# Optimization experiments

Hardware: AMD Instinct MI355X
Metric: run time of the kernel (lower is better)

Reference implementation:

```python
import jax, jax.numpy as jnp
import numpy as np

IN_DIM = 4096
OUT_DIM = 4096
RANK = 16
BATCH = 4
SEQ = 2048


def setup_inputs() -> dict:
    key = jax.random.key(0)
    ks = jax.random.split(key, 7)
    x = jax.random.normal(ks[0], (BATCH, SEQ, IN_DIM), dtype=jnp.float32)
    org_weight = jax.random.normal(ks[1], (OUT_DIM, IN_DIM), dtype=jnp.float32) * 0.02
    org_bias = jax.random.normal(ks[2], (OUT_DIM,), dtype=jnp.float32) * 0.02
    hada_w1_a = jax.random.normal(ks[3], (OUT_DIM, RANK), dtype=jnp.float32) * 0.1
    hada_w1_b = jax.random.normal(ks[4], (RANK, IN_DIM), dtype=jnp.float32)
    hada_w2_a = jax.random.normal(ks[5], (OUT_DIM, RANK), dtype=jnp.float32) * 0.1
    hada_w2_b = jax.random.normal(ks[6], (RANK, IN_DIM), dtype=jnp.float32)
    scalar = jnp.ones((), dtype=jnp.float32)
    return {
        "x": x,
        "org_weight": org_weight,
        "org_bias": org_bias,
        "hada_w1_a": hada_w1_a,
        "hada_w1_b": hada_w1_b,
        "hada_w2_a": hada_w2_a,
        "hada_w2_b": hada_w2_b,
        "scalar": scalar,
    }


def reference(x, org_weight, org_bias, hada_w1_a, hada_w1_b, hada_w2_a, hada_w2_b, scalar):
    scale = jnp.asarray(1.0, dtype=hada_w1_b.dtype)   # self.scale = 1.0
    multiplier = jnp.asarray(1.0, dtype=x.dtype)       # self.multiplier = 1.0
    # base = F.linear(x, org_weight, org_bias)
    base = jnp.einsum("bsi,oi->bso", x, org_weight) + org_bias
    # diff_weight = (w1a @ w1b) * (w2a @ w2b) * scale * scalar  -> [out, in]
    diff_weight = (hada_w1_a @ hada_w1_b) * (hada_w2_a @ hada_w2_b) * scale * scalar
    # delta = F.linear(x, diff_weight * multiplier)
    delta = jnp.einsum("bsi,oi->bso", x, diff_weight * multiplier)
    return base + delta
```

## Files before the change

### kernel.cpp

```cpp
#include <hip/hip_runtime.h>

#define IN_DIM 4096
#define OUT_DIM 4096
#define RANK 16
#define MDIM 8192

typedef unsigned short ushort_t;
typedef __attribute__((ext_vector_type(8))) short short8;
typedef __attribute__((ext_vector_type(4))) float floatx4;
typedef __attribute__((ext_vector_type(4))) ushort_t ushort4_t;

__device__ __forceinline__ ushort_t f2b(float f) {
    union { float f; unsigned int i; } v; v.f = f;
    unsigned int u = v.i;
    u += 0x7FFFu + ((u >> 16) & 1u);
    return (ushort_t)(u >> 16);
}

#define GLOAD_LDS16(gp, lp)                                                    \
    __builtin_amdgcn_global_load_lds(                                          \
        (__attribute__((address_space(1))) void*)(gp),                         \
        (__attribute__((address_space(3))) void*)(lp), 16, 0, 0)

__global__ __launch_bounds__(256) void convx_kernel(
    const float4* __restrict__ x, ushort4_t* __restrict__ xb, int n4)
{
    int i = blockIdx.x * blockDim.x + threadIdx.x;
    int stride = gridDim.x * blockDim.x;
    for (; i < n4; i += stride) {
        float4 v = x[i];
        ushort4_t o;
        o.x = f2b(v.x); o.y = f2b(v.y); o.z = f2b(v.z); o.w = f2b(v.w);
        xb[i] = o;
    }
}

__global__ __launch_bounds__(256) void weff_kernel(
    const float* __restrict__ orgw,
    const float* __restrict__ w1a, const float* __restrict__ w1b,
    const float* __restrict__ w2a, const float* __restrict__ w2b,
    const float* __restrict__ scalar,
    ushort_t* __restrict__ weff)
{
    __shared__ float s1b[RANK][256];
    __shared__ float s2b[RANK][256];
    __shared__ float s1a[64 * RANK];
    __shared__ float s2a[64 * RANK];

    const int t  = threadIdx.x;
    const int i0 = blockIdx.x * 256;
    const int o0 = blockIdx.y * 64;

    #pragma unroll
    for (int r = 0; r < RANK; ++r) {
        s1b[r][t] = w1b[r * IN_DIM + i0 + t];
        s2b[r][t] = w2b[r * IN_DIM + i0 + t];
    }
    for (int e = t; e < 64 * RANK; e += 256) {
        s1a[e] = w1a[o0 * RANK + e];
        s2a[e] = w2a[o0 * RANK + e];
    }
    __syncthreads();

    const float sc = scalar[0];
    for (int o = 0; o < 64; ++o) {
        float a1 = 0.f, a2 = 0.f;
        #pragma unroll
        for (int r = 0; r < RANK; ++r) {
            a1 += s1a[o * RANK + r] * s1b[r][t];
            a2 += s2a[o * RANK + r] * s2b[r][t];
        }
        const int idx = (o0 + o) * IN_DIM + i0 + t;
        weff[idx] = f2b(orgw[idx] + a1 * a2 * sc);
    }
}

#define BM 128
#define BN 128
#define BK 32

__global__ __launch_bounds__(256) void gemm_kernel(
    const ushort_t* __restrict__ X,
    const ushort_t* __restrict__ W,
    const float* __restrict__ bias,
    float* __restrict__ out)
{
    __shared__ __align__(16) short lA[BM * BK];
    __shared__ __align__(16) short lB[BN * BK];

    const int t    = threadIdx.x;
    const int w    = t >> 6;
    const int lane = t & 63;
    const int m0   = blockIdx.y * BM;
    const int n0   = blockIdx.x * BN;

    const int quad  = lane >> 4;
    const int r16   = lane & 15;
    const int mrow0 = (w >> 1) * 64;
    const int ncol0 = (w & 1) * 64;

    const int c0  = w * 128 + lane;
    const int c1  = c0 + 64;
    const int rA0 = c0 >> 2, kA0 = c0 & 3;
    const int rA1 = c1 >> 2, kA1 = c1 & 3;
    const ushort_t* gA0 = X + (size_t)(m0 + rA0) * IN_DIM + kA0 * 8;
    const ushort_t* gA1 = X + (size_t)(m0 + rA1) * IN_DIM + kA1 * 8;
    const ushort_t* gB0 = W + (size_t)(n0 + rA0) * IN_DIM + kA0 * 8;
    const ushort_t* gB1 = W + (size_t)(n0 + rA1) * IN_DIM + kA1 * 8;
    short* lA0 = &lA[(w * 128) * 8];
    short* lA1 = &lA[(w * 128 + 64) * 8];
    short* lB0 = &lB[(w * 128) * 8];
    short* lB1 = &lB[(w * 128 + 64) * 8];

    const short* pA = &lA[(mrow0 + r16) * BK + quad * 8];
    const short* pB = &lB[(ncol0 + r16) * BK + quad * 8];

    floatx4 acc[4][4];
    #pragma unroll
    for (int i = 0; i < 4; ++i)
        #pragma unroll
        for (int j = 0; j < 4; ++j)
            acc[i][j] = (floatx4){0.f, 0.f, 0.f, 0.f};

    for (int it = 0; it < IN_DIM / BK; ++it) {
        const int k0 = it * BK;
        __syncthreads();
        GLOAD_LDS16(gA0 + k0, lA0);
        GLOAD_LDS16(gA1 + k0, lA1);
        GLOAD_LDS16(gB0 + k0, lB0);
        GLOAD_LDS16(gB1 + k0, lB1);
        __syncthreads();

        short8 af[4], bfr[4];
        #pragma unroll
        for (int i = 0; i < 4; ++i) {
            af[i]  = *(const short8*)(pA + i * 16 * BK);
            bfr[i] = *(const short8*)(pB + i * 16 * BK);
        }
        #pragma unroll
        for (int mi = 0; mi < 4; ++mi)
            #pragma unroll
            for (int ni = 0; ni < 4; ++ni)
                acc[mi][ni] = __builtin_amdgcn_mfma_f32_16x16x32_bf16(
                    af[mi], bfr[ni], acc[mi][ni], 0, 0, 0);
    }

    #pragma unroll
    for (int ni = 0; ni < 4; ++ni) {
        const int gn = n0 + ncol0 + ni * 16 + r16;
        const float bv = bias[gn];
        #pragma unroll
        for (int mi = 0; mi < 4; ++mi) {
            const int gmb = m0 + mrow0 + mi * 16 + quad * 4;
            #pragma unroll
            for (int rr = 0; rr < 4; ++rr) {
                out[(size_t)(gmb + rr) * OUT_DIM + gn] = acc[mi][ni][rr] + bv;
            }
        }
    }
}

extern "C" void kernel_launch(void* const* d_in, const int* in_sizes, int n_in,
                              void* d_out, int out_size, void* d_ws, size_t ws_size,
                              hipStream_t stream) {
    const float* x      = (const float*)d_in[0];
    const float* orgw   = (const float*)d_in[1];
    const float* bias   = (const float*)d_in[2];
    const float* w1a    = (const float*)d_in[3];
    const float* w1b    = (const float*)d_in[4];
    const float* w2a    = (const float*)d_in[5];
    const float* w2b    = (const float*)d_in[6];
    const float* scalar = (const float*)d_in[7];

    ushort_t* xb   = (ushort_t*)d_ws;
    ushort_t* weff = (ushort_t*)d_ws + (size_t)MDIM * IN_DIM;
    float* out = (float*)d_out;

    const int n4 = MDIM * IN_DIM / 4;
    convx_kernel<<<2048, 256, 0, stream>>>((const float4*)x, (ushort4_t*)xb, n4);
    weff_kernel<<<dim3(IN_DIM / 256, OUT_DIM / 64), 256, 0, stream>>>(
        orgw, w1a, w1b, w2a, w2b, scalar, weff);
    gemm_kernel<<<dim3(OUT_DIM / BN, MDIM / BM), 256, 0, stream>>>(
        xb, weff, bias, out);
}
```

Baseline: 610.8 us.

## Rewrite bf16 GEMM as 256x256 double-buffered pipelined kernel with swizzled LDS

Replaces the single-buffered 128x128x32 GEMM with a 256x256x64 tile kernel using 512 threads, double-buffered LDS, XOR-swizzled LDS layout, and interleaved global->LDS staging between MFMA phases with s_setprio. It also adds a block-id swizzle for L2 locality. The goal is to hide global load latency, cut LDS bank conflicts and raise arithmetic intensity per block. It costs much higher register and LDS pressure (128 accumulators per thread, 128KB LDS), which may limit occupancy.

```diff
diff --git a/kernel.cpp b/kernel.cpp
--- a/kernel.cpp
+++ b/kernel.cpp
@@ -75,87 +75,188 @@
     }
 }
 
-#define BM 128
-#define BN 128
-#define BK 32
-
-__global__ __launch_bounds__(256) void gemm_kernel(
+#define BM 256
+#define BN 256
+#define BK 64
+
+#define STAGE_A(buf, half, kcol)                                               \
+    do {                                                                       \
+        GLOAD_LDS16(gX0 + (size_t)(half) * (128 * IN_DIM) + (kcol),            \
+                    (short*)&lA[buf][half][0][0] + w * 512);                   \
+        GLOAD_LDS16(gX1 + (size_t)(half) * (128 * IN_DIM) + (kcol),            \
+                    (short*)&lA[buf][half][0][0] + 4096 + w * 512);            \
+    } while (0)
+
+#define STAGE_B(buf, half, kcol)                                               \
+    do {                                                                       \
+        GLOAD_LDS16(gW0 + (size_t)(half) * (128 * IN_DIM) + (kcol),            \
+                    (short*)&lB[buf][half][0][0] + w * 512);                   \
+        GLOAD_LDS16(gW1 + (size_t)(half) * (128 * IN_DIM) + (kcol),            \
+                    (short*)&lB[buf][half][0][0] + 4096 + w * 512);            \
+    } while (0)
+
+#define MFMA_(d, a, b) (d) = __builtin_amdgcn_mfma_f32_16x16x32_bf16((a), (b), (d), 0, 0, 0)
+
+#define HALF_ITER(aB, bB, S1, S2, S3, S4)                                      \
+    do {                                                                       \
+        short8 a_lo[4][2], a_hi[4][2], b_lo[2][2], b_hi[2][2];                 \
+                         \
+        _Pragma("unroll")                                                      \
+        for (int mi = 0; mi < 4; ++mi) {                                       \
+            a_lo[mi][0] = *(const short8*)((aB) + mi * 1024 + ok0);            \
+            a_lo[mi][1] = *(const short8*)((aB) + mi * 1024 + ok1);            \
+        }                                                                      \
+        _Pragma("unroll")                                                      \
+        for (int ni = 0; ni < 2; ++ni) {                                       \
+            b_lo[ni][0] = *(const short8*)((bB) + ni * 1024 + ok0);            \
+            b_lo[ni][1] = *(const short8*)((bB) + ni * 1024 + ok1);            \
+        }                                                                      \
+        S1;                                                                    \
+        __builtin_amdgcn_s_barrier();                                          \
+        asm volatile("s_waitcnt lgkmcnt(0)" ::: "memory");                     \
+        __builtin_amdgcn_s_setprio(1);                                         \
+        _Pragma("unroll")                                                      \
+        for (int mi = 0; mi < 4; ++mi)                                         \
+            _Pragma("unroll")                                                  \
+            for (int ni = 0; ni < 2; ++ni) {                                   \
+                MFMA_(acc[mi][ni], a_lo[mi][0], b_lo[ni][0]);                  \
+                MFMA_(acc[mi][ni], a_lo[mi][1], b_lo[ni][1]);                  \
+            }                                                                  \
+        __builtin_amdgcn_s_setprio(0);                                         \
+        __builtin_amdgcn_s_barrier();                                          \
+                                 \
+        _Pragma("unroll")                                                      \
+        for (int mi = 0; mi < 4; ++mi) {                                       \
+            a_hi[mi][0] = *(const short8*)((aB) + 4096 + mi * 1024 + ok0);     \
+            a_hi[mi][1] = *(const short8*)((aB) + 4096 + mi * 1024 + ok1);     \
+        }                                                                      \
+        S2;                                                                    \
+        __builtin_amdgcn_s_barrier();                                          \
+        asm volatile("s_waitcnt lgkmcnt(0)" ::: "memory");                     \
+        __builtin_amdgcn_s_setprio(1);                                         \
+        _Pragma("unroll")                                                      \
+        for (int mi = 0; mi < 4; ++mi)                                         \
+            _Pragma("unroll")                                                  \
+            for (int ni = 0; ni < 2; ++ni) {                                   \
+                MFMA_(acc[4 + mi][ni], a_hi[mi][0], b_lo[ni][0]);              \
+                MFMA_(acc[4 + mi][ni], a_hi[mi][1], b_lo[ni][1]);              \
+            }                                                                  \
+        __builtin_amdgcn_s_setprio(0);                                         \
+        __builtin_amdgcn_s_barrier();                                          \
+                                 \
+        _Pragma("unroll")                                                      \
+        for (int ni = 0; ni < 2; ++ni) {                                       \
+            b_hi[ni][0] = *(const short8*)((bB) + 2048 + ni * 1024 + ok0);     \
+            b_hi[ni][1] = *(const short8*)((bB) + 2048 + ni * 1024 + ok1);     \
+        }                                                                      \
+        S3;                                                                    \
+        __builtin_amdgcn_s_barrier();                                          \
+        asm volatile("s_waitcnt lgkmcnt(0)" ::: "memory");                     \
+        __builtin_amdgcn_s_setprio(1);                                         \
+        _Pragma("unroll")                                                      \
+        for (int mi = 0; mi < 4; ++mi)                                         \
+            _Pragma("unroll")                                                  \
+            for (int ni = 0; ni < 2; ++ni) {                                   \
+                MFMA_(acc[4 + mi][2 + ni], a_hi[mi][0], b_hi[ni][0]);          \
+                MFMA_(acc[4 + mi][2 + ni], a_hi[mi][1], b_hi[ni][1]);          \
+            }                                                                  \
+        __builtin_amdgcn_s_setprio(0);                                         \
+        __builtin_amdgcn_s_barrier();                                          \
+           \
+        S4;                                                                    \
+        __builtin_amdgcn_s_barrier();                                          \
+        __builtin_amdgcn_s_setprio(1);                                         \
+        _Pragma("unroll")                                                      \
+        for (int mi = 0; mi < 4; ++mi)                                         \
+            _Pragma("unroll")                                                  \
+            for (int ni = 0; ni < 2; ++ni) {                                   \
+                MFMA_(acc[mi][2 + ni], a_lo[mi][0], b_hi[ni][0]);              \
+                MFMA_(acc[mi][2 + ni], a_lo[mi][1], b_hi[ni][1]);              \
+            }                                                                  \
+        __builtin_amdgcn_s_setprio(0);                                         \
+        asm volatile("s_waitcnt vmcnt(4)" ::: "memory");                       \
+        __builtin_amdgcn_s_barrier();                                          \
+    } while (0)
+
+__global__ __launch_bounds__(512, 2) void gemm_kernel(
     const ushort_t* __restrict__ X,
     const ushort_t* __restrict__ W,
     const float* __restrict__ bias,
     float* __restrict__ out)
 {
-    __shared__ __align__(16) short lA[BM * BK];
-    __shared__ __align__(16) short lB[BN * BK];
+    __shared__ __align__(16) short lA[2][2][128][64];
+    __shared__ __align__(16) short lB[2][2][128][64];
 
     const int t    = threadIdx.x;
     const int w    = t >> 6;
     const int lane = t & 63;
-    const int m0   = blockIdx.y * BM;
-    const int n0   = blockIdx.x * BN;
-
-    const int quad  = lane >> 4;
-    const int r16   = lane & 15;
-    const int mrow0 = (w >> 1) * 64;
-    const int ncol0 = (w & 1) * 64;
-
-    const int c0  = w * 128 + lane;
-    const int c1  = c0 + 64;
-    const int rA0 = c0 >> 2, kA0 = c0 & 3;
-    const int rA1 = c1 >> 2, kA1 = c1 & 3;
-    const ushort_t* gA0 = X + (size_t)(m0 + rA0) * IN_DIM + kA0 * 8;
-    const ushort_t* gA1 = X + (size_t)(m0 + rA1) * IN_DIM + kA1 * 8;
-    const ushort_t* gB0 = W + (size_t)(n0 + rA0) * IN_DIM + kA0 * 8;
-    const ushort_t* gB1 = W + (size_t)(n0 + rA1) * IN_DIM + kA1 * 8;
-    short* lA0 = &lA[(w * 128) * 8];
-    short* lA1 = &lA[(w * 128 + 64) * 8];
-    short* lB0 = &lB[(w * 128) * 8];
-    short* lB1 = &lB[(w * 128 + 64) * 8];
-
-    const short* pA = &lA[(mrow0 + r16) * BK + quad * 8];
-    const short* pB = &lB[(ncol0 + r16) * BK + quad * 8];
-
-    floatx4 acc[4][4];
+    const int quad = lane >> 4;
+    const int r16  = lane & 15;
+    const int wm   = w >> 2;
+    const int wn   = w & 3;
+
+    const int bid = blockIdx.y * gridDim.x + blockIdx.x;
+    const int swz = (bid & 7) * 64 + (bid >> 3);
+    const int m0  = (swz >> 4) * BM;
+    const int n0  = (swz & 15) * BN;
+
+    const int s0  = w * 64 + lane;
+    const int s1  = 512 + s0;
+    const int r0  = s0 >> 3, r1 = s1 >> 3;
+    const int k80 = (s0 & 7) ^ (r0 & 7);
+    const int k81 = (s1 & 7) ^ (r1 & 7);
+    const ushort_t* gX0 = X + (size_t)(m0 + r0) * IN_DIM + k80 * 8;
+    const ushort_t* gX1 = X + (size_t)(m0 + r1) * IN_DIM + k81 * 8;
+    const ushort_t* gW0 = W + (size_t)(n0 + r0) * IN_DIM + k80 * 8;
+    const ushort_t* gW1 = W + (size_t)(n0 + r1) * IN_DIM + k81 * 8;
+
+    const short* aB0 = &lA[0][wm][r16][0];
+    const short* aB1 = &lA[1][wm][r16][0];
+    const short* bB0 = &lB[0][wn >> 1][(wn & 1) * 64 + r16][0];
+    const short* bB1 = &lB[1][wn >> 1][(wn & 1) * 64 + r16][0];
+    const int ok0 = ((0 + quad) ^ (r16 & 7)) << 3;
+    const int ok1 = ((4 + quad) ^ (r16 & 7)) << 3;
+
+    floatx4 acc[8][4];
     #pragma unroll
-    for (int i = 0; i < 4; ++i)
+    for (int i = 0; i < 8; ++i)
         #pragma unroll
         for (int j = 0; j < 4; ++j)
             acc[i][j] = (floatx4){0.f, 0.f, 0.f, 0.f};
 
-    for (int it = 0; it < IN_DIM / BK; ++it) {
-        const int k0 = it * BK;
-        __syncthreads();
-        GLOAD_LDS16(gA0 + k0, lA0);
-        GLOAD_LDS16(gA1 + k0, lA1);
-        GLOAD_LDS16(gB0 + k0, lB0);
-        GLOAD_LDS16(gB1 + k0, lB1);
-        __syncthreads();
-
-        short8 af[4], bfr[4];
-        #pragma unroll
-        for (int i = 0; i < 4; ++i) {
-            af[i]  = *(const short8*)(pA + i * 16 * BK);
-            bfr[i] = *(const short8*)(pB + i * 16 * BK);
-        }
-        #pragma unroll
-        for (int mi = 0; mi < 4; ++mi)
-            #pragma unroll
-            for (int ni = 0; ni < 4; ++ni)
-                acc[mi][ni] = __builtin_amdgcn_mfma_f32_16x16x32_bf16(
-                    af[mi], bfr[ni], acc[mi][ni], 0, 0, 0);
+    STAGE_A(0, 0, 0);
+    STAGE_A(0, 1, 0);
+    STAGE_B(0, 0, 0);
+    STAGE_B(0, 1, 0);
+    STAGE_A(1, 0, 64);
+    STAGE_A(1, 1, 64);
+    asm volatile("s_waitcnt vmcnt(4)" ::: "memory");
+    __builtin_amdgcn_s_barrier();
+
+    for (int it = 0; it < IN_DIM / 128; ++it) {
+        const int kmax = IN_DIM - 64;
+        int kB1 = it * 128 + 64;  if (kB1 > kmax) kB1 = kmax;
+        int kA2 = it * 128 + 128; if (kA2 > kmax) kA2 = kmax;
+        int kA3 = it * 128 + 192; if (kA3 > kmax) kA3 = kmax;
+
+        HALF_ITER(aB0, bB0,
+                  STAGE_B(1, 0, kB1), STAGE_B(1, 1, kB1),
+                  STAGE_A(0, 0, kA2), STAGE_A(0, 1, kA2));
+        HALF_ITER(aB1, bB1,
+                  STAGE_B(0, 0, kA2), STAGE_B(0, 1, kA2),
+                  STAGE_A(1, 0, kA3), STAGE_A(1, 1, kA3));
     }
 
     #pragma unroll
     for (int ni = 0; ni < 4; ++ni) {
-        const int gn = n0 + ncol0 + ni * 16 + r16;
+        const int gn = n0 + wn * 64 + ni * 16 + r16;
         const float bv = bias[gn];
         #pragma unroll
-        for (int mi = 0; mi < 4; ++mi) {
-            const int gmb = m0 + mrow0 + mi * 16 + quad * 4;
+        for (int mi = 0; mi < 8; ++mi) {
+            const int gm = m0 + wm * 128 + mi * 16 + quad * 4;
             #pragma unroll
-            for (int rr = 0; rr < 4; ++rr) {
-                out[(size_t)(gmb + rr) * OUT_DIM + gn] = acc[mi][ni][rr] + bv;
-            }
+            for (int rr = 0; rr < 4; ++rr)
+                out[(size_t)(gm + rr) * OUT_DIM + gn] = acc[mi][ni][rr] + bv;
         }
     }
 }
@@ -180,6 +281,6 @@
     convx_kernel<<<2048, 256, 0, stream>>>((const float4*)x, (ushort4_t*)xb, n4);
     weff_kernel<<<dim3(IN_DIM / 256, OUT_DIM / 64), 256, 0, stream>>>(
         orgw, w1a, w1b, w2a, w2b, scalar, weff);
-    gemm_kernel<<<dim3(OUT_DIM / BN, MDIM / BM), 256, 0, stream>>>(
+    gemm_kernel<<<dim3(OUT_DIM / BN, MDIM / BM), 512, 0, stream>>>(
         xb, weff, bias, out);
 }
```

Result: faster. 598.4 us (-2.0%).
